# Kernel optimization log

Measured on AMD Instinct MI355X. Metric: run time of the kernel, lower is better.

Reference implementation:

```python
import jax, jax.numpy as jnp
import numpy as np

A_BITS = 16
W_BITS = 8
KH = KW = 3
STRIDE = 1
PADDING = 1


def fake_quant(x, bits, axes=None):
    """Asymmetric min/max fake quantization with straight-through estimator."""
    if axes is None:
        mn = x.min()
        mx = x.max()
    else:
        mn = x.min(axis=axes, keepdims=True)
        mx = x.max(axis=axes, keepdims=True)
    qmax = float(2 ** bits - 1)
    scale = jnp.maximum((mx - mn) / qmax, 1e-12)
    zp = jnp.round(-mn / scale)
    q = jnp.clip(jnp.round(x / scale) + zp, 0.0, qmax)
    deq = (q - zp) * scale
    # STE: identity gradient through the quantizer
    return x + jax.lax.stop_gradient(deq - x)


def unfold(x, kh, kw, stride, padding):
    """torch.nn.functional.unfold equivalent -> (N, C*kh*kw, Hout*Wout)."""
    N, C, H, W = x.shape
    xp = jnp.pad(x, ((0, 0), (0, 0), (padding, padding), (padding, padding)))
    Ho = (H - kh + 2 * padding) // stride + 1
    Wo = (W - kw + 2 * padding) // stride + 1
    cols = []
    for i in range(kh):          # small fixed 3x3 loop
        for j in range(kw):
            cols.append(xp[:, :, i:i + Ho * stride:stride, j:j + Wo * stride:stride])
    xcol = jnp.stack(cols, axis=2)              # (N, C, kh*kw, Ho, Wo)
    return xcol.reshape(N, C * kh * kw, Ho * Wo), Ho, Wo


def adder_op(W_col, X_col):
    # W_col: (F, K), X_col: (K, L) -> out: (F, L); L1-distance "conv"
    return -jnp.abs(W_col[:, :, None] - X_col[None, :, :]).sum(axis=1)


def setup_inputs() -> dict:
    key = jax.random.key(0)
    kx, kw = jax.random.split(key)
    x = jax.random.normal(kx, (4, 64, 28, 28), dtype=jnp.float32)
    W = jax.random.normal(kw, (64, 64, 3, 3), dtype=jnp.float32)
    return {"x": x, "W": W}


def reference(x, W):
    # first_layer == 0 -> activation fake-quant; per-channel weight fake-quant
    qx = fake_quant(x, A_BITS)
    qw = fake_quant(W, W_BITS, axes=(1, 2, 3))
    N = x.shape[0]
    F = W.shape[0]
    xcol, Ho, Wo = unfold(qx, KH, KW, STRIDE, PADDING)   # (N, K, L0)
    K = xcol.shape[1]
    # torch: permute(1,2,0).view(K, L0*N) -> batch fastest within a row
    X_col = jnp.transpose(xcol, (1, 2, 0)).reshape(K, -1)  # (K, L0*N)
    W_col = qw.reshape(F, K)
    out = adder_op(W_col, X_col)                            # (F, L0*N)
    out = out.reshape(F, Ho, Wo, N).transpose(3, 0, 1, 2)   # (N, F, Ho, Wo)
    return out
```

## Files before the change

### kernel.cpp

```cpp
#include <hip/hip_runtime.h>
#include <math.h>

#define N_  4
#define C_  64
#define H_  28
#define W_  28
#define F_  64
#define KK  576
#define NX  (N_*C_*H_*W_)
#define NX4 (NX/4)


__global__ __launch_bounds__(256) void k_minmax(const float* __restrict__ x,
                                                float* __restrict__ ws) {
  __shared__ float sm[4], sM[4];
  int tid = threadIdx.x;
  int gid = blockIdx.x * 256 + tid;
  const float4* x4 = (const float4*)x;
  float m = 3.4e38f, M = -3.4e38f;
  for (int i = gid; i < NX4; i += 64 * 256) {
    float4 v = x4[i];
    m = fminf(m, fminf(fminf(v.x, v.y), fminf(v.z, v.w)));
    M = fmaxf(M, fmaxf(fmaxf(v.x, v.y), fmaxf(v.z, v.w)));
  }
  #pragma unroll
  for (int o = 32; o; o >>= 1) {
    m = fminf(m, __shfl_xor(m, o));
    M = fmaxf(M, __shfl_xor(M, o));
  }
  if ((tid & 63) == 0) { sm[tid >> 6] = m; sM[tid >> 6] = M; }
  __syncthreads();
  if (tid == 0) {
    m = fminf(fminf(sm[0], sm[1]), fminf(sm[2], sm[3]));
    M = fmaxf(fmaxf(sM[0], sM[1]), fmaxf(sM[2], sM[3]));
    ws[blockIdx.x] = m;
    ws[64 + blockIdx.x] = M;
  }
}

__global__ __launch_bounds__(256) void k_main(const float* __restrict__ x,
                                              const float* __restrict__ Wg,
                                              const float* __restrict__ ws,
                                              float* __restrict__ out) {
  __shared__ __align__(16) float Xs[64 * 3 * 32];
  __shared__ __align__(16) float Wl[KK * 33];
  int tid  = threadIdx.x;
  int lane = tid & 63, wv = tid >> 6;
  int y = blockIdx.x, n = blockIdx.y, fh = blockIdx.z;

  float m = ws[lane], M = ws[64 + lane];
  #pragma unroll
  for (int o = 32; o; o >>= 1) {
    m = fminf(m, __shfl_xor(m, o));
    M = fmaxf(M, __shfl_xor(M, o));
  }
  float sx = fmaxf((M - m) / 65535.0f, 1e-12f);
  float zx = rintf(-m / sx);

  for (int idx = tid; idx < 64 * 3 * 30; idx += 256) {
    int c = idx / 90, rem = idx - c * 90;
    int r = rem / 30, p = rem - r * 30;
    int row = y + r - 1, col = p - 1;
    float v = 0.0f;
    if ((unsigned)row < 28u && (unsigned)col < 28u) {
      float raw = x[((n * 64 + c) * 28 + row) * 28 + col];
      float q = fminf(fmaxf(rintf(raw / sx) + zx, 0.0f), 65535.0f);
      v = (q - zx) * sx;
    }
    Xs[(c * 3 + r) * 32 + p] = v;
  }

  for (int t = 0; t < 8; ++t) {
    int fl = wv * 8 + t;
    int fg = fh * 32 + fl;
    const float* wp = Wg + fg * KK;
    float v[9];
    float wm = 3.4e38f, wM = -3.4e38f;
    #pragma unroll
    for (int u = 0; u < 9; ++u) {
      v[u] = wp[lane + 64 * u];
      wm = fminf(wm, v[u]);
      wM = fmaxf(wM, v[u]);
    }
    #pragma unroll
    for (int o = 32; o; o >>= 1) {
      wm = fminf(wm, __shfl_xor(wm, o));
      wM = fmaxf(wM, __shfl_xor(wM, o));
    }
    float s = fmaxf((wM - wm) / 255.0f, 1e-12f);
    float z = rintf(-wm / s);
    #pragma unroll
    for (int u = 0; u < 9; ++u) {
      float q = fminf(fmaxf(rintf(v[u] / s) + z, 0.0f), 255.0f);
      Wl[(lane + 64 * u) * 33 + fl] = (q - z) * s;
    }
  }

  __syncthreads();

  int fl = tid & 31, g = tid >> 5;
  int base = g * 4;
  bool active = (base < 28);
  float acc0 = 0.f, acc1 = 0.f, acc2 = 0.f, acc3 = 0.f;

  if (active) {
    const float* xb = &Xs[base];
    const float* wb = &Wl[fl];
    for (int c = 0; c < 64; ++c) {
      const float* xr = xb + c * 96;
      float4 a0 = *(const float4*)(xr);
      float4 a1 = *(const float4*)(xr + 4);
      float4 b0 = *(const float4*)(xr + 32);
      float4 b1 = *(const float4*)(xr + 36);
      float4 c0 = *(const float4*)(xr + 64);
      float4 c1 = *(const float4*)(xr + 68);
      const float* wr = wb + c * 297;
      float w0 = wr[0],   w1 = wr[33],  w2 = wr[66];
      float w3 = wr[99],  w4 = wr[132], w5 = wr[165];
      float w6 = wr[198], w7 = wr[231], w8 = wr[264];

      acc0 += fabsf(w0 - a0.x) + fabsf(w1 - a0.y) + fabsf(w2 - a0.z)
            + fabsf(w3 - b0.x) + fabsf(w4 - b0.y) + fabsf(w5 - b0.z)
            + fabsf(w6 - c0.x) + fabsf(w7 - c0.y) + fabsf(w8 - c0.z);
      acc1 += fabsf(w0 - a0.y) + fabsf(w1 - a0.z) + fabsf(w2 - a0.w)
            + fabsf(w3 - b0.y) + fabsf(w4 - b0.z) + fabsf(w5 - b0.w)
            + fabsf(w6 - c0.y) + fabsf(w7 - c0.z) + fabsf(w8 - c0.w);
      acc2 += fabsf(w0 - a0.z) + fabsf(w1 - a0.w) + fabsf(w2 - a1.x)
            + fabsf(w3 - b0.z) + fabsf(w4 - b0.w) + fabsf(w5 - b1.x)
            + fabsf(w6 - c0.z) + fabsf(w7 - c0.w) + fabsf(w8 - c1.x);
      acc3 += fabsf(w0 - a0.w) + fabsf(w1 - a1.x) + fabsf(w2 - a1.y)
            + fabsf(w3 - b0.w) + fabsf(w4 - b1.x) + fabsf(w5 - b1.y)
            + fabsf(w6 - c0.w) + fabsf(w7 - c1.x) + fabsf(w8 - c1.y);
    }
    int f = fh * 32 + fl;
    float4* o = (float4*)(out + ((n * 64 + f) * 28 + y) * 28 + base);
    *o = make_float4(-acc0, -acc1, -acc2, -acc3);
  }
}

extern "C" void kernel_launch(void* const* d_in, const int* in_sizes, int n_in,
                              void* d_out, int out_size, void* d_ws, size_t ws_size,
                              hipStream_t stream) {
  const float* x  = (const float*)d_in[0];
  const float* Wg = (const float*)d_in[1];
  float* out = (float*)d_out;
  float* ws  = (float*)d_ws;

  hipLaunchKernelGGL(k_minmax, dim3(64), dim3(256), 0, stream, x, ws);
  hipLaunchKernelGGL(k_main, dim3(28, 4, 2), dim3(256), 0, stream, x, Wg, ws, out);
}
```

Measured before the change: 90.40 us.

## Quantize weights once in prep kernel and load transposed weights into main kernel

Weight fake-quantization, including the per-filter min/max reductions, moves out of every main-kernel block (224 blocks each redoing 32 filters) into the first 16 blocks of the prep kernel. The prep kernel writes the result to workspace transposed as [k][f]. The main kernel now only copies its half of that table into shared memory with float4 loads. Divisions by the scale are replaced with multiplication by a reciprocal, and the channel loop gets unroll 2. The reciprocal can change rounding slightly versus the reference's true division.

```diff
diff --git a/kernel.cpp b/kernel.cpp
--- a/kernel.cpp
+++ b/kernel.cpp
@@ -11,14 +11,15 @@
 #define NX4 (NX/4)
 
 
-__global__ __launch_bounds__(256) void k_minmax(const float* __restrict__ x,
-                                                float* __restrict__ ws) {
+__global__ __launch_bounds__(256) void k_prep(const float* __restrict__ x,
+                                              const float* __restrict__ Wg,
+                                              float* __restrict__ ws) {
   __shared__ float sm[4], sM[4];
-  int tid = threadIdx.x;
-  int gid = blockIdx.x * 256 + tid;
+  int tid = threadIdx.x, lane = tid & 63, wv = tid >> 6;
+
   const float4* x4 = (const float4*)x;
   float m = 3.4e38f, M = -3.4e38f;
-  for (int i = gid; i < NX4; i += 64 * 256) {
+  for (int i = blockIdx.x * 256 + tid; i < NX4; i += 64 * 256) {
     float4 v = x4[i];
     m = fminf(m, fminf(fminf(v.x, v.y), fminf(v.z, v.w)));
     M = fmaxf(M, fmaxf(fmaxf(v.x, v.y), fmaxf(v.z, v.w)));
@@ -28,7 +29,7 @@
     m = fminf(m, __shfl_xor(m, o));
     M = fmaxf(M, __shfl_xor(M, o));
   }
-  if ((tid & 63) == 0) { sm[tid >> 6] = m; sM[tid >> 6] = M; }
+  if (lane == 0) { sm[wv] = m; sM[wv] = M; }
   __syncthreads();
   if (tid == 0) {
     m = fminf(fminf(sm[0], sm[1]), fminf(sm[2], sm[3]));
@@ -36,44 +37,10 @@
     ws[blockIdx.x] = m;
     ws[64 + blockIdx.x] = M;
   }
-}
 
-__global__ __launch_bounds__(256) void k_main(const float* __restrict__ x,
-                                              const float* __restrict__ Wg,
-                                              const float* __restrict__ ws,
-                                              float* __restrict__ out) {
-  __shared__ __align__(16) float Xs[64 * 3 * 32];
-  __shared__ __align__(16) float Wl[KK * 33];
-  int tid  = threadIdx.x;
-  int lane = tid & 63, wv = tid >> 6;
-  int y = blockIdx.x, n = blockIdx.y, fh = blockIdx.z;
-
-  float m = ws[lane], M = ws[64 + lane];
-  #pragma unroll
-  for (int o = 32; o; o >>= 1) {
-    m = fminf(m, __shfl_xor(m, o));
-    M = fmaxf(M, __shfl_xor(M, o));
-  }
-  float sx = fmaxf((M - m) / 65535.0f, 1e-12f);
-  float zx = rintf(-m / sx);
-
-  for (int idx = tid; idx < 64 * 3 * 30; idx += 256) {
-    int c = idx / 90, rem = idx - c * 90;
-    int r = rem / 30, p = rem - r * 30;
-    int row = y + r - 1, col = p - 1;
-    float v = 0.0f;
-    if ((unsigned)row < 28u && (unsigned)col < 28u) {
-      float raw = x[((n * 64 + c) * 28 + row) * 28 + col];
-      float q = fminf(fmaxf(rintf(raw / sx) + zx, 0.0f), 65535.0f);
-      v = (q - zx) * sx;
-    }
-    Xs[(c * 3 + r) * 32 + p] = v;
-  }
-
-  for (int t = 0; t < 8; ++t) {
-    int fl = wv * 8 + t;
-    int fg = fh * 32 + fl;
-    const float* wp = Wg + fg * KK;
+  if (blockIdx.x < 16) {
+    int f = blockIdx.x * 4 + wv;
+    const float* wp = Wg + f * KK;
     float v[9];
     float wm = 3.4e38f, wM = -3.4e38f;
     #pragma unroll
@@ -89,10 +56,57 @@
     }
     float s = fmaxf((wM - wm) / 255.0f, 1e-12f);
     float z = rintf(-wm / s);
+    float rs = 1.0f / s;
+    float* Wt = ws + 256;
     #pragma unroll
     for (int u = 0; u < 9; ++u) {
-      float q = fminf(fmaxf(rintf(v[u] / s) + z, 0.0f), 255.0f);
-      Wl[(lane + 64 * u) * 33 + fl] = (q - z) * s;
+      float q = fminf(fmaxf(rintf(v[u] * rs) + z, 0.0f), 255.0f);
+      Wt[(lane + 64 * u) * 64 + f] = (q - z) * s;
+    }
+  }
+}
+
+__global__ __launch_bounds__(256) void k_main(const float* __restrict__ x,
+                                              const float* __restrict__ ws,
+                                              float* __restrict__ out) {
+  __shared__ __align__(16) float Xs[64 * 3 * 32];
+  __shared__ __align__(16) float Wl[KK * 33];
+  int tid  = threadIdx.x;
+  int lane = tid & 63;
+  int y = blockIdx.x, n = blockIdx.y, fh = blockIdx.z;
+
+  float m = ws[lane], M = ws[64 + lane];
+  #pragma unroll
+  for (int o = 32; o; o >>= 1) {
+    m = fminf(m, __shfl_xor(m, o));
+    M = fmaxf(M, __shfl_xor(M, o));
+  }
+  float sx = fmaxf((M - m) / 65535.0f, 1e-12f);
+  float zx = rintf(-m / sx);
+  float rx = 1.0f / sx;
+
+  for (int idx = tid; idx < 64 * 3 * 30; idx += 256) {
+    int c = idx / 90, rem = idx - c * 90;
+    int r = rem / 30, p = rem - r * 30;
+    int row = y + r - 1, col = p - 1;
+    float v = 0.0f;
+    if ((unsigned)row < 28u && (unsigned)col < 28u) {
+      float raw = x[((n * 64 + c) * 28 + row) * 28 + col];
+      float q = fminf(fmaxf(rintf(raw * rx) + zx, 0.0f), 65535.0f);
+      v = (q - zx) * sx;
+    }
+    Xs[(c * 3 + r) * 32 + p] = v;
+  }
+
+  {
+    const float4* Wt4 = (const float4*)(ws + 256);
+    #pragma unroll
+    for (int i = 0; i < 18; ++i) {
+      int idx = tid + 256 * i;
+      int k = idx >> 3, q = idx & 7;
+      float4 v = Wt4[k * 16 + fh * 8 + q];
+      float* d = &Wl[k * 33 + q * 4];
+      d[0] = v.x; d[1] = v.y; d[2] = v.z; d[3] = v.w;
     }
   }
 
@@ -106,6 +120,7 @@
   if (active) {
     const float* xb = &Xs[base];
     const float* wb = &Wl[fl];
+    #pragma unroll 2
     for (int c = 0; c < 64; ++c) {
       const float* xr = xb + c * 96;
       float4 a0 = *(const float4*)(xr);
@@ -146,6 +161,6 @@
   float* out = (float*)d_out;
   float* ws  = (float*)d_ws;
 
-  hipLaunchKernelGGL(k_minmax, dim3(64), dim3(256), 0, stream, x, ws);
-  hipLaunchKernelGGL(k_main, dim3(28, 4, 2), dim3(256), 0, stream, x, Wg, ws, out);
+  hipLaunchKernelGGL(k_prep, dim3(64), dim3(256), 0, stream, x, Wg, ws);
+  hipLaunchKernelGGL(k_main, dim3(28, 4, 2), dim3(256), 0, stream, x, ws, out);
 }
```

Result: faster. 85.48 us (-5.4%).
